# Kernel optimization log

Measured on AMD Instinct MI355X. Metric: run time of the kernel, lower is better.

Reference implementation:

```python
import jax, jax.numpy as jnp
import numpy as np

N = 6144
IN_DIM = 256
HID = 64
HEADS = 4
LAT = 32
ALPHA = 0.2  # LeakyReLU negative slope
NEG_INF = -9e15


def setup_inputs() -> dict:
    key = jax.random.key(0)
    ks = jax.random.split(key, 6)
    x = jax.random.normal(ks[0], (N, IN_DIM), jnp.float32)
    # sparse symmetric 0/1 adjacency, avg degree ~ 25
    A = (jax.random.uniform(ks[1], (N, N)) < 0.004).astype(jnp.float32)
    A = jnp.maximum(A, A.T)
    # xavier-uniform-ish params, matching pyGAT GraphAttentionLayer shapes
    s1 = float(np.sqrt(6.0 / (IN_DIM + HID)))
    W_heads = jax.random.uniform(ks[2], (HEADS, IN_DIM, HID), jnp.float32, -s1, s1)
    sa = float(np.sqrt(6.0 / (2 * HID + 1)))
    a_heads = jax.random.uniform(ks[3], (HEADS, 2 * HID), jnp.float32, -sa, sa)
    s2 = float(np.sqrt(6.0 / (HEADS * HID + LAT)))
    W_out = jax.random.uniform(ks[4], (HEADS * HID, LAT), jnp.float32, -s2, s2)
    sb = float(np.sqrt(6.0 / (2 * LAT + 1)))
    a_out = jax.random.uniform(ks[5], (2 * LAT,), jnp.float32, -sb, sb)
    return {"x": x, "A": A, "W_heads": W_heads, "a_heads": a_heads,
            "W_out": W_out, "a_out": a_out}


def _gat_layer(h, adj_mask, W, a, concat):
    # h: [N, F_in], W: [F_in, F], a: [2F]
    Wh = h @ W                              # [N, F]
    f = W.shape[1]
    e_src = Wh @ a[:f]                      # [N]
    e_dst = Wh @ a[f:]                      # [N]
    e = jax.nn.leaky_relu(e_src[:, None] + e_dst[None, :], ALPHA)  # [N, N]
    e = jnp.where(adj_mask, e, NEG_INF)
    att = jax.nn.softmax(e, axis=1)         # masked softmax over neighbors
    out = att @ Wh                          # [N, F]
    return jax.nn.elu(out) if concat else out


def reference(x, A, W_heads, a_heads, W_out, a_out):
    # normalize(A, 'sym', False): D^{-1/2} A D^{-1/2}
    deg = A.sum(axis=1)
    dinv = jnp.where(deg > 0, deg ** -0.5, 0.0)
    An = A * dinv[:, None] * dinv[None, :]
    mask = An > 0
    heads = [_gat_layer(x, mask, W_heads[i], a_heads[i], True) for i in range(HEADS)]
    h = jnp.concatenate(heads, axis=1)      # [N, HEADS*HID]
    z = jax.nn.elu(_gat_layer(h, mask, W_out, a_out, False))  # [N, LAT]
    return jax.nn.sigmoid(z @ z.T)          # [N, N]
```

## Files before the change

### kernel.cpp

```cpp
#include <hip/hip_runtime.h>
#include <hip/hip_bf16.h>

#define NN 6144
#define IN_DIM 256
#define HID 64
#define HEADS 4
#define LAT 32
#define CAP 192
#define ALPHA 0.2f
#define GEMM_BLOCKS 384

typedef __attribute__((ext_vector_type(8))) short bf16x8;
typedef __attribute__((ext_vector_type(4))) float f32x4;

__device__ __forceinline__ float elu_f(float v)   { return v > 0.f ? v : expm1f(v); }
__device__ __forceinline__ float lrelu_f(float v) { return v > 0.f ? v : ALPHA * v; }

__device__ __forceinline__ void split_bf16(float v, unsigned short& hi, unsigned short& lo) {
    unsigned u = __builtin_bit_cast(unsigned, v);
    hi = (unsigned short)(u >> 16);
    float vh = __builtin_bit_cast(float, u & 0xFFFF0000u);
    float rl = v - vh;
    lo = (unsigned short)(__builtin_bit_cast(unsigned, rl) >> 16);
}
__device__ __forceinline__ unsigned short f2bf(float f) {
    unsigned u = __builtin_bit_cast(unsigned, f);
    return (unsigned short)((u + 0x7FFFu + ((u >> 16) & 1u)) >> 16);
}
__device__ __forceinline__ float bf2f(unsigned short b) {
    return __builtin_bit_cast(float, (unsigned)b << 16);
}

__global__ __launch_bounds__(256) void k_pre(const float* __restrict__ A,
                                             const float* __restrict__ x,
                                             const float* __restrict__ Wheads,
                                             const float* __restrict__ aheads,
                                             int* __restrict__ nbr, int* __restrict__ cnt,
                                             unsigned short* __restrict__ Whb,
                                             float* __restrict__ es, float* __restrict__ ed) {
    __shared__ __align__(16) float smem[2048];
    int bid = blockIdx.x;
    int t = threadIdx.x;
    if (bid < GEMM_BLOCKS) {
        int head = bid & 3, m0 = (bid >> 2) * 64;
        float (*As)[64] = (float(*)[64])smem;
        float (*Bs)[64] = (float(*)[64])(smem + 1024);
        const float* Wc = Wheads + (size_t)head * IN_DIM * HID;
        int ty = t >> 4, tx = t & 15;
        float acc[4][4] = {};
        for (int k0 = 0; k0 < IN_DIM; k0 += 16) {
            {
                int row = t >> 2, k4 = (t & 3) * 4;
                float4 v = *(const float4*)(x + (size_t)(m0 + row) * IN_DIM + k0 + k4);
                As[k4 + 0][row] = v.x; As[k4 + 1][row] = v.y;
                As[k4 + 2][row] = v.z; As[k4 + 3][row] = v.w;
                int kk = t >> 4, n4 = (t & 15) * 4;
                *(float4*)&Bs[kk][n4] = *(const float4*)(Wc + (size_t)(k0 + kk) * HID + n4);
            }
            __syncthreads();
            #pragma unroll
            for (int k = 0; k < 16; ++k) {
                float4 av = *(float4*)&As[k][ty * 4];
                float4 bv = *(float4*)&Bs[k][tx * 4];
                float ar[4] = {av.x, av.y, av.z, av.w};
                float br[4] = {bv.x, bv.y, bv.z, bv.w};
                #pragma unroll
                for (int i = 0; i < 4; ++i)
                    #pragma unroll
                    for (int j = 0; j < 4; ++j)
                        acc[i][j] = fmaf(ar[i], br[j], acc[i][j]);
            }
            __syncthreads();
        }
        #pragma unroll
        for (int i = 0; i < 4; ++i) {
            ushort4 o;
            o.x = f2bf(acc[i][0]); o.y = f2bf(acc[i][1]);
            o.z = f2bf(acc[i][2]); o.w = f2bf(acc[i][3]);
            *(ushort4*)(Whb + (size_t)(m0 + ty * 4 + i) * (HEADS * HID) + head * HID + tx * 4) = o;
        }
        float4 a1v = *(const float4*)(aheads + head * 2 * HID + tx * 4);
        float4 a2v = *(const float4*)(aheads + head * 2 * HID + HID + tx * 4);
        #pragma unroll
        for (int i = 0; i < 4; ++i) {
            float p1 = acc[i][0] * a1v.x + acc[i][1] * a1v.y + acc[i][2] * a1v.z + acc[i][3] * a1v.w;
            float p2 = acc[i][0] * a2v.x + acc[i][1] * a2v.y + acc[i][2] * a2v.z + acc[i][3] * a2v.w;
            #pragma unroll
            for (int off = 8; off; off >>= 1) {
                p1 += __shfl_down(p1, off, 16);
                p2 += __shfl_down(p2, off, 16);
            }
            if (tx == 0) {
                es[head * NN + m0 + ty * 4 + i] = p1;
                ed[head * NN + m0 + ty * 4 + i] = p2;
            }
        }
    } else {
        int row = bid - GEMM_BLOCKS;
        int* lcnt = (int*)smem;
        const float4* Arow = (const float4*)(A + (size_t)row * NN);
        if (t == 0) *lcnt = 0;
        __syncthreads();
        int* my = nbr + (size_t)row * CAP;
        #pragma unroll
        for (int it = 0; it < NN / 4 / 256; ++it) {
            int idx4 = it * 256 + t;
            float4 v = Arow[idx4];
            int base = idx4 * 4;
            if (v.x != 0.f) { int p = atomicAdd(lcnt, 1); if (p < CAP) my[p] = base; }
            if (v.y != 0.f) { int p = atomicAdd(lcnt, 1); if (p < CAP) my[p] = base + 1; }
            if (v.z != 0.f) { int p = atomicAdd(lcnt, 1); if (p < CAP) my[p] = base + 2; }
            if (v.w != 0.f) { int p = atomicAdd(lcnt, 1); if (p < CAP) my[p] = base + 3; }
        }
        __syncthreads();
        if (t == 0) cnt[row] = *lcnt < CAP ? *lcnt : CAP;
    }
}

__global__ __launch_bounds__(256, 8) void k_attn1g2(const int* __restrict__ nbr, const int* __restrict__ cnt,
                                                    const float* __restrict__ es, const float* __restrict__ ed,
                                                    const unsigned short* __restrict__ Whb,
                                                    const float* __restrict__ Wout, const float* __restrict__ aout,
                                                    float* __restrict__ Wh2,
                                                    float* __restrict__ es2, float* __restrict__ ed2) {
    __shared__ int col[CAP];
    __shared__ float att[HEADS][CAP];
    __shared__ float hrow[HEADS * HID];
    __shared__ float part[8][LAT];
    int i = blockIdx.x;
    int t = threadIdx.x, h = t >> 6, l = t & 63;
    int c = cnt[i];
    float hval;
    if (c == 0) {
        float s = 0.f;
        for (int r = 0; r < NN; ++r) s += bf2f(Whb[(size_t)r * (HEADS * HID) + h * HID + l]);
        hval = elu_f(s * (1.0f / NN));
    } else {
        const int* nb = nbr + (size_t)i * CAP;
        float esi = es[h * NN + i];
        float m = -3.0e38f;
        for (int j = l; j < c; j += 64) {
            int cj = nb[j];
            if (h == 0) col[j] = cj;
            float e = lrelu_f(esi + ed[h * NN + cj]);
            att[h][j] = e;
            m = fmaxf(m, e);
        }
        #pragma unroll
        for (int off = 32; off; off >>= 1) m = fmaxf(m, __shfl_down(m, off));
        m = __shfl(m, 0);
        float s = 0.f;
        for (int j = l; j < c; j += 64) {
            float p = __expf(att[h][j] - m);
            att[h][j] = p;
            s += p;
        }
        #pragma unroll
        for (int off = 32; off; off >>= 1) s += __shfl_down(s, off);
        s = __shfl(s, 0);
        __syncthreads();
        float inv = 1.0f / s;
        const unsigned short* WhH = Whb + h * HID + l;
        float a0 = 0.f, a1 = 0.f, a2 = 0.f, a3 = 0.f;
        float a4 = 0.f, a5 = 0.f, a6 = 0.f, a7 = 0.f;
        int j = 0;
        for (; j + 8 <= c; j += 8) {
            a0 = fmaf(att[h][j + 0], bf2f(WhH[(size_t)col[j + 0] * (HEADS * HID)]), a0);
            a1 = fmaf(att[h][j + 1], bf2f(WhH[(size_t)col[j + 1] * (HEADS * HID)]), a1);
            a2 = fmaf(att[h][j + 2], bf2f(WhH[(size_t)col[j + 2] * (HEADS * HID)]), a2);
            a3 = fmaf(att[h][j + 3], bf2f(WhH[(size_t)col[j + 3] * (HEADS * HID)]), a3);
            a4 = fmaf(att[h][j + 4], bf2f(WhH[(size_t)col[j + 4] * (HEADS * HID)]), a4);
            a5 = fmaf(att[h][j + 5], bf2f(WhH[(size_t)col[j + 5] * (HEADS * HID)]), a5);
            a6 = fmaf(att[h][j + 6], bf2f(WhH[(size_t)col[j + 6] * (HEADS * HID)]), a6);
            a7 = fmaf(att[h][j + 7], bf2f(WhH[(size_t)col[j + 7] * (HEADS * HID)]), a7);
        }
        for (; j < c; ++j)
            a0 = fmaf(att[h][j], bf2f(WhH[(size_t)col[j] * (HEADS * HID)]), a0);
        hval = elu_f((((a0 + a1) + (a2 + a3)) + ((a4 + a5) + (a6 + a7))) * inv);
    }
    hrow[h * HID + l] = hval;
    __syncthreads();
    {
        int half = l >> 5, cc = l & 31;
        int tbase = h * HID + half * 32;
        float p = 0.f;
        #pragma unroll 8
        for (int tt = 0; tt < 32; ++tt)
            p = fmaf(hrow[tbase + tt], Wout[(tbase + tt) * LAT + cc], p);
        part[h * 2 + half][cc] = p;
    }
    __syncthreads();
    if (t < 32) {
        float acc = 0.f;
        #pragma unroll
        for (int w = 0; w < 8; ++w) acc += part[w][t];
        Wh2[(size_t)i * LAT + t] = acc;
        float p1 = acc * aout[t], p2 = acc * aout[LAT + t];
        #pragma unroll
        for (int off = 16; off; off >>= 1) {
            p1 += __shfl_down(p1, off, 32);
            p2 += __shfl_down(p2, off, 32);
        }
        if (t == 0) { es2[i] = p1; ed2[i] = p2; }
    }
}

__global__ __launch_bounds__(256, 8) void k_attn2(const int* __restrict__ nbr, const int* __restrict__ cnt,
                                                  const float* __restrict__ es2, const float* __restrict__ ed2,
                                                  const float* __restrict__ Wh2,
                                                  unsigned short* __restrict__ zh, unsigned short* __restrict__ zl) {
    __shared__ float att[4][CAP];
    __shared__ int col[4][CAP];
    int w = threadIdx.x >> 6, l = threadIdx.x & 63;
    int i = blockIdx.x * 4 + w;
    int c = cnt[i];
    if (c == 0) {
        if (l < LAT) {
            float s = 0.f;
            for (int r = 0; r < NN; ++r) s += Wh2[(size_t)r * LAT + l];
            unsigned short hi, lo;
            split_bf16(elu_f(s * (1.0f / NN)), hi, lo);
            zh[(size_t)i * LAT + l] = hi;
            zl[(size_t)i * LAT + l] = lo;
        }
        return;
    }
    float esi = es2[i];
    const int* nb = nbr + (size_t)i * CAP;
    float m = -3.0e38f;
    for (int j = l; j < c; j += 64) {
        int cj = nb[j];
        col[w][j] = cj;
        float e = lrelu_f(esi + ed2[cj]);
        att[w][j] = e;
        m = fmaxf(m, e);
    }
    #pragma unroll
    for (int off = 32; off; off >>= 1) m = fmaxf(m, __shfl_down(m, off));
    m = __shfl(m, 0);
    float s = 0.f;
    for (int j = l; j < c; j += 64) {
        float p = __expf(att[w][j] - m);
        att[w][j] = p;
        s += p;
    }
    #pragma unroll
    for (int off = 32; off; off >>= 1) s += __shfl_down(s, off);
    s = __shfl(s, 0);
    if (l < LAT) {
        float inv = 1.0f / s;
        float a0 = 0.f, a1 = 0.f, a2 = 0.f, a3 = 0.f;
        int j = 0;
        for (; j + 4 <= c; j += 4) {
            a0 = fmaf(att[w][j + 0], Wh2[(size_t)col[w][j + 0] * LAT + l], a0);
            a1 = fmaf(att[w][j + 1], Wh2[(size_t)col[w][j + 1] * LAT + l], a1);
            a2 = fmaf(att[w][j + 2], Wh2[(size_t)col[w][j + 2] * LAT + l], a2);
            a3 = fmaf(att[w][j + 3], Wh2[(size_t)col[w][j + 3] * LAT + l], a3);
        }
        for (; j < c; ++j)
            a0 = fmaf(att[w][j], Wh2[(size_t)col[w][j] * LAT + l], a0);
        unsigned short hi, lo;
        split_bf16(elu_f(((a0 + a1) + (a2 + a3)) * inv), hi, lo);
        zh[(size_t)i * LAT + l] = hi;
        zl[(size_t)i * LAT + l] = lo;
    }
}

__global__ __launch_bounds__(256, 8) void k_zzt(const unsigned short* __restrict__ zh,
                                                const unsigned short* __restrict__ zl,
                                                float* __restrict__ out) {
    int t = threadIdx.x, w = t >> 6, l = t & 63;
    int m0 = blockIdx.y * 64 + w * 16;
    int n0 = blockIdx.x * 64;
    int r = l & 15, kg = (l >> 4) * 8;
    bf16x8 ah = *(const bf16x8*)(zh + (size_t)(m0 + r) * LAT + kg);
    bf16x8 al = *(const bf16x8*)(zl + (size_t)(m0 + r) * LAT + kg);
    int mbase = m0 + (l >> 4) * 4;
    #pragma unroll
    for (int jp = 0; jp < 2; ++jp) {
        int nbA = n0 + (jp * 2 + 0) * 16;
        int nbB = n0 + (jp * 2 + 1) * 16;
        bf16x8 bhA = *(const bf16x8*)(zh + (size_t)(nbA + r) * LAT + kg);
        bf16x8 blA = *(const bf16x8*)(zl + (size_t)(nbA + r) * LAT + kg);
        bf16x8 bhB = *(const bf16x8*)(zh + (size_t)(nbB + r) * LAT + kg);
        bf16x8 blB = *(const bf16x8*)(zl + (size_t)(nbB + r) * LAT + kg);
        f32x4 accA = {0.f, 0.f, 0.f, 0.f};
        accA = __builtin_amdgcn_mfma_f32_16x16x32_bf16(ah, bhA, accA, 0, 0, 0);
        accA = __builtin_amdgcn_mfma_f32_16x16x32_bf16(ah, blA, accA, 0, 0, 0);
        accA = __builtin_amdgcn_mfma_f32_16x16x32_bf16(al, bhA, accA, 0, 0, 0);
        f32x4 accB = {0.f, 0.f, 0.f, 0.f};
        accB = __builtin_amdgcn_mfma_f32_16x16x32_bf16(ah, bhB, accB, 0, 0, 0);
        accB = __builtin_amdgcn_mfma_f32_16x16x32_bf16(ah, blB, accB, 0, 0, 0);
        accB = __builtin_amdgcn_mfma_f32_16x16x32_bf16(al, bhB, accB, 0, 0, 0);
        float4 oA, oB;
        oA.x = 1.0f / (1.0f + __expf(-accA[0]));
        oA.y = 1.0f / (1.0f + __expf(-accA[1]));
        oA.z = 1.0f / (1.0f + __expf(-accA[2]));
        oA.w = 1.0f / (1.0f + __expf(-accA[3]));
        oB.x = 1.0f / (1.0f + __expf(-accB[0]));
        oB.y = 1.0f / (1.0f + __expf(-accB[1]));
        oB.z = 1.0f / (1.0f + __expf(-accB[2]));
        oB.w = 1.0f / (1.0f + __expf(-accB[3]));
        *(float4*)(out + (size_t)(nbA + (l & 15)) * NN + mbase) = oA;
        *(float4*)(out + (size_t)(nbB + (l & 15)) * NN + mbase) = oB;
    }
}

extern "C" void kernel_launch(void* const* d_in, const int* in_sizes, int n_in,
                              void* d_out, int out_size, void* d_ws, size_t ws_size,
                              hipStream_t stream) {
    const float* x      = (const float*)d_in[0];
    const float* A      = (const float*)d_in[1];
    const float* Wheads = (const float*)d_in[2];
    const float* aheads = (const float*)d_in[3];
    const float* Wout   = (const float*)d_in[4];
    const float* aout   = (const float*)d_in[5];
    float* out = (float*)d_out;

    char* ws = (char*)d_ws;
    size_t o = 0;
    auto alloc = [&](size_t bytes) { void* p = ws + o; o += (bytes + 255) & ~(size_t)255; return p; };
    int*   nbr   = (int*)  alloc((size_t)NN * CAP * 4);
    int*   cnt   = (int*)  alloc((size_t)NN * 4);
    unsigned short* Whb = (unsigned short*)alloc((size_t)NN * HEADS * HID * 2);
    float* es    = (float*)alloc((size_t)HEADS * NN * 4);
    float* ed    = (float*)alloc((size_t)HEADS * NN * 4);
    float* Wh2   = (float*)alloc((size_t)NN * LAT * 4);
    float* es2   = (float*)alloc((size_t)NN * 4);
    float* ed2   = (float*)alloc((size_t)NN * 4);
    unsigned short* zh = (unsigned short*)alloc((size_t)NN * LAT * 2);
    unsigned short* zl = (unsigned short*)alloc((size_t)NN * LAT * 2);

    k_pre     <<<GEMM_BLOCKS + NN, 256, 0, stream>>>(A, x, Wheads, aheads, nbr, cnt, Whb, es, ed);
    k_attn1g2 <<<NN, 256, 0, stream>>>(nbr, cnt, es, ed, Whb, Wout, aout, Wh2, es2, ed2);
    k_attn2   <<<NN / 4, 256, 0, stream>>>(nbr, cnt, es2, ed2, Wh2, zh, zl);
    k_zzt     <<<dim3(NN / 64, NN / 64), 256, 0, stream>>>(zh, zl, out);
}
```

Measured before the change: 115.4 us.

## Process one node per wavefront in layer-1 attention with interleaved head scores

The es/ed attention scores are now stored node-major with all four heads together, so one float4 load fetches every head's score for a neighbour. The layer-1 attention kernel now gives each wavefront a whole node (four nodes per block) rather than one block per node. Each lane gathers four consecutive bf16 features per neighbour with a ushort4 load, and the cross-block partial-sum stage for the Wout projection becomes a wave shuffle. This cuts per-node synchronisation and the number of gather instructions, at the cost of a serial 128-term Wout dot product per lane and more shared memory per block.

```diff
diff --git a/kernel.cpp b/kernel.cpp
--- a/kernel.cpp
+++ b/kernel.cpp
@@ -37,7 +37,7 @@
                                              const float* __restrict__ aheads,
                                              int* __restrict__ nbr, int* __restrict__ cnt,
                                              unsigned short* __restrict__ Whb,
-                                             float* __restrict__ es, float* __restrict__ ed) {
+                                             float* __restrict__ es4, float* __restrict__ ed4) {
     __shared__ __align__(16) float smem[2048];
     int bid = blockIdx.x;
     int t = threadIdx.x;
@@ -91,8 +91,8 @@
                 p2 += __shfl_down(p2, off, 16);
             }
             if (tx == 0) {
-                es[head * NN + m0 + ty * 4 + i] = p1;
-                ed[head * NN + m0 + ty * 4 + i] = p2;
+                es4[(size_t)(m0 + ty * 4 + i) * 4 + head] = p1;
+                ed4[(size_t)(m0 + ty * 4 + i) * 4 + head] = p2;
             }
         }
     } else {
@@ -118,90 +118,112 @@
 }
 
 __global__ __launch_bounds__(256, 8) void k_attn1g2(const int* __restrict__ nbr, const int* __restrict__ cnt,
-                                                    const float* __restrict__ es, const float* __restrict__ ed,
+                                                    const float4* __restrict__ es4, const float4* __restrict__ ed4,
                                                     const unsigned short* __restrict__ Whb,
                                                     const float* __restrict__ Wout, const float* __restrict__ aout,
                                                     float* __restrict__ Wh2,
                                                     float* __restrict__ es2, float* __restrict__ ed2) {
-    __shared__ int col[CAP];
-    __shared__ float att[HEADS][CAP];
-    __shared__ float hrow[HEADS * HID];
-    __shared__ float part[8][LAT];
-    int i = blockIdx.x;
-    int t = threadIdx.x, h = t >> 6, l = t & 63;
+    __shared__ int colS[4][CAP];
+    __shared__ __align__(16) float att4[4][CAP][4];
+    __shared__ __align__(16) float hrow[4][HEADS * HID];
+    int w = threadIdx.x >> 6, l = threadIdx.x & 63;
+    int i = blockIdx.x * 4 + w;
     int c = cnt[i];
-    float hval;
+    const int* nb = nbr + (size_t)i * CAP;
+
+    float4 esv = es4[i];
+    float m0 = -3.0e38f, m1 = -3.0e38f, m2 = -3.0e38f, m3 = -3.0e38f;
+    for (int j = l; j < c; j += 64) {
+        int cj = nb[j];
+        colS[w][j] = cj;
+        float4 edv = ed4[cj];
+        float4 e;
+        e.x = lrelu_f(esv.x + edv.x); e.y = lrelu_f(esv.y + edv.y);
+        e.z = lrelu_f(esv.z + edv.z); e.w = lrelu_f(esv.w + edv.w);
+        *(float4*)&att4[w][j][0] = e;
+        m0 = fmaxf(m0, e.x); m1 = fmaxf(m1, e.y);
+        m2 = fmaxf(m2, e.z); m3 = fmaxf(m3, e.w);
+    }
+    #pragma unroll
+    for (int off = 32; off; off >>= 1) {
+        m0 = fmaxf(m0, __shfl_down(m0, off)); m1 = fmaxf(m1, __shfl_down(m1, off));
+        m2 = fmaxf(m2, __shfl_down(m2, off)); m3 = fmaxf(m3, __shfl_down(m3, off));
+    }
+    m0 = __shfl(m0, 0); m1 = __shfl(m1, 0); m2 = __shfl(m2, 0); m3 = __shfl(m3, 0);
+    float s0 = 0.f, s1 = 0.f, s2 = 0.f, s3 = 0.f;
+    for (int j = l; j < c; j += 64) {
+        float4 e = *(float4*)&att4[w][j][0];
+        e.x = __expf(e.x - m0); e.y = __expf(e.y - m1);
+        e.z = __expf(e.z - m2); e.w = __expf(e.w - m3);
+        *(float4*)&att4[w][j][0] = e;
+        s0 += e.x; s1 += e.y; s2 += e.z; s3 += e.w;
+    }
+    #pragma unroll
+    for (int off = 32; off; off >>= 1) {
+        s0 += __shfl_down(s0, off); s1 += __shfl_down(s1, off);
+        s2 += __shfl_down(s2, off); s3 += __shfl_down(s3, off);
+    }
+    s0 = __shfl(s0, 0); s1 = __shfl(s1, 0); s2 = __shfl(s2, 0); s3 = __shfl(s3, 0);
+    __syncthreads();
+
+    int hd = l >> 4;
+    float sh = hd < 2 ? (hd == 0 ? s0 : s1) : (hd == 2 ? s2 : s3);
+    float invh = 1.0f / sh;
+    float4 hv;
     if (c == 0) {
-        float s = 0.f;
-        for (int r = 0; r < NN; ++r) s += bf2f(Whb[(size_t)r * (HEADS * HID) + h * HID + l]);
-        hval = elu_f(s * (1.0f / NN));
+        float a0 = 0.f, a1 = 0.f, a2 = 0.f, a3 = 0.f;
+        for (int r = 0; r < NN; ++r) {
+            ushort4 v = *(const ushort4*)(Whb + (size_t)r * (HEADS * HID) + 4 * l);
+            a0 += bf2f(v.x); a1 += bf2f(v.y); a2 += bf2f(v.z); a3 += bf2f(v.w);
+        }
+        hv.x = elu_f(a0 / NN); hv.y = elu_f(a1 / NN);
+        hv.z = elu_f(a2 / NN); hv.w = elu_f(a3 / NN);
     } else {
-        const int* nb = nbr + (size_t)i * CAP;
-        float esi = es[h * NN + i];
-        float m = -3.0e38f;
-        for (int j = l; j < c; j += 64) {
-            int cj = nb[j];
-            if (h == 0) col[j] = cj;
-            float e = lrelu_f(esi + ed[h * NN + cj]);
-            att[h][j] = e;
-            m = fmaxf(m, e);
-        }
-        #pragma unroll
-        for (int off = 32; off; off >>= 1) m = fmaxf(m, __shfl_down(m, off));
-        m = __shfl(m, 0);
-        float s = 0.f;
-        for (int j = l; j < c; j += 64) {
-            float p = __expf(att[h][j] - m);
-            att[h][j] = p;
-            s += p;
-        }
-        #pragma unroll
-        for (int off = 32; off; off >>= 1) s += __shfl_down(s, off);
-        s = __shfl(s, 0);
-        __syncthreads();
-        float inv = 1.0f / s;
-        const unsigned short* WhH = Whb + h * HID + l;
-        float a0 = 0.f, a1 = 0.f, a2 = 0.f, a3 = 0.f;
-        float a4 = 0.f, a5 = 0.f, a6 = 0.f, a7 = 0.f;
+        const unsigned short* Wb = Whb + 4 * l;
+        float aA0 = 0.f, aA1 = 0.f, aA2 = 0.f, aA3 = 0.f;
+        float aB0 = 0.f, aB1 = 0.f, aB2 = 0.f, aB3 = 0.f;
         int j = 0;
-        for (; j + 8 <= c; j += 8) {
-            a0 = fmaf(att[h][j + 0], bf2f(WhH[(size_t)col[j + 0] * (HEADS * HID)]), a0);
-            a1 = fmaf(att[h][j + 1], bf2f(WhH[(size_t)col[j + 1] * (HEADS * HID)]), a1);
-            a2 = fmaf(att[h][j + 2], bf2f(WhH[(size_t)col[j + 2] * (HEADS * HID)]), a2);
-            a3 = fmaf(att[h][j + 3], bf2f(WhH[(size_t)col[j + 3] * (HEADS * HID)]), a3);
-            a4 = fmaf(att[h][j + 4], bf2f(WhH[(size_t)col[j + 4] * (HEADS * HID)]), a4);
-            a5 = fmaf(att[h][j + 5], bf2f(WhH[(size_t)col[j + 5] * (HEADS * HID)]), a5);
-            a6 = fmaf(att[h][j + 6], bf2f(WhH[(size_t)col[j + 6] * (HEADS * HID)]), a6);
-            a7 = fmaf(att[h][j + 7], bf2f(WhH[(size_t)col[j + 7] * (HEADS * HID)]), a7);
-        }
-        for (; j < c; ++j)
-            a0 = fmaf(att[h][j], bf2f(WhH[(size_t)col[j] * (HEADS * HID)]), a0);
-        hval = elu_f((((a0 + a1) + (a2 + a3)) + ((a4 + a5) + (a6 + a7))) * inv);
-    }
-    hrow[h * HID + l] = hval;
+        for (; j + 2 <= c; j += 2) {
+            int cjA = colS[w][j], cjB = colS[w][j + 1];
+            float fA = att4[w][j][hd], fB = att4[w][j + 1][hd];
+            ushort4 vA = *(const ushort4*)(Wb + (size_t)cjA * (HEADS * HID));
+            ushort4 vB = *(const ushort4*)(Wb + (size_t)cjB * (HEADS * HID));
+            aA0 = fmaf(fA, bf2f(vA.x), aA0); aA1 = fmaf(fA, bf2f(vA.y), aA1);
+            aA2 = fmaf(fA, bf2f(vA.z), aA2); aA3 = fmaf(fA, bf2f(vA.w), aA3);
+            aB0 = fmaf(fB, bf2f(vB.x), aB0); aB1 = fmaf(fB, bf2f(vB.y), aB1);
+            aB2 = fmaf(fB, bf2f(vB.z), aB2); aB3 = fmaf(fB, bf2f(vB.w), aB3);
+        }
+        if (j < c) {
+            int cj = colS[w][j];
+            float f = att4[w][j][hd];
+            ushort4 v = *(const ushort4*)(Wb + (size_t)cj * (HEADS * HID));
+            aA0 = fmaf(f, bf2f(v.x), aA0); aA1 = fmaf(f, bf2f(v.y), aA1);
+            aA2 = fmaf(f, bf2f(v.z), aA2); aA3 = fmaf(f, bf2f(v.w), aA3);
+        }
+        hv.x = elu_f((aA0 + aB0) * invh); hv.y = elu_f((aA1 + aB1) * invh);
+        hv.z = elu_f((aA2 + aB2) * invh); hv.w = elu_f((aA3 + aB3) * invh);
+    }
+    *(float4*)&hrow[w][4 * l] = hv;
     __syncthreads();
+
     {
         int half = l >> 5, cc = l & 31;
-        int tbase = h * HID + half * 32;
+        int tbase = half * 128;
         float p = 0.f;
         #pragma unroll 8
-        for (int tt = 0; tt < 32; ++tt)
-            p = fmaf(hrow[tbase + tt], Wout[(tbase + tt) * LAT + cc], p);
-        part[h * 2 + half][cc] = p;
-    }
-    __syncthreads();
-    if (t < 32) {
-        float acc = 0.f;
-        #pragma unroll
-        for (int w = 0; w < 8; ++w) acc += part[w][t];
-        Wh2[(size_t)i * LAT + t] = acc;
-        float p1 = acc * aout[t], p2 = acc * aout[LAT + t];
-        #pragma unroll
-        for (int off = 16; off; off >>= 1) {
-            p1 += __shfl_down(p1, off, 32);
-            p2 += __shfl_down(p2, off, 32);
-        }
-        if (t == 0) { es2[i] = p1; ed2[i] = p2; }
+        for (int tt = 0; tt < 128; ++tt)
+            p = fmaf(hrow[w][tbase + tt], Wout[(tbase + tt) * LAT + cc], p);
+        p += __shfl_down(p, 32);
+        if (l < 32) {
+            Wh2[(size_t)i * LAT + cc] = p;
+            float p1 = p * aout[cc], p2 = p * aout[LAT + cc];
+            #pragma unroll
+            for (int off = 16; off; off >>= 1) {
+                p1 += __shfl_down(p1, off, 32);
+                p2 += __shfl_down(p2, off, 32);
+            }
+            if (cc == 0) { es2[i] = p1; ed2[i] = p2; }
+        }
     }
 }
 
@@ -323,16 +345,17 @@
     int*   nbr   = (int*)  alloc((size_t)NN * CAP * 4);
     int*   cnt   = (int*)  alloc((size_t)NN * 4);
     unsigned short* Whb = (unsigned short*)alloc((size_t)NN * HEADS * HID * 2);
-    float* es    = (float*)alloc((size_t)HEADS * NN * 4);
-    float* ed    = (float*)alloc((size_t)HEADS * NN * 4);
+    float* es4   = (float*)alloc((size_t)NN * 4 * 4);
+    float* ed4   = (float*)alloc((size_t)NN * 4 * 4);
     float* Wh2   = (float*)alloc((size_t)NN * LAT * 4);
     float* es2   = (float*)alloc((size_t)NN * 4);
     float* ed2   = (float*)alloc((size_t)NN * 4);
     unsigned short* zh = (unsigned short*)alloc((size_t)NN * LAT * 2);
     unsigned short* zl = (unsigned short*)alloc((size_t)NN * LAT * 2);
 
-    k_pre     <<<GEMM_BLOCKS + NN, 256, 0, stream>>>(A, x, Wheads, aheads, nbr, cnt, Whb, es, ed);
-    k_attn1g2 <<<NN, 256, 0, stream>>>(nbr, cnt, es, ed, Whb, Wout, aout, Wh2, es2, ed2);
+    k_pre     <<<GEMM_BLOCKS + NN, 256, 0, stream>>>(A, x, Wheads, aheads, nbr, cnt, Whb, es4, ed4);
+    k_attn1g2 <<<NN / 4, 256, 0, stream>>>(nbr, cnt, (const float4*)es4, (const float4*)ed4,
+                                           Whb, Wout, aout, Wh2, es2, ed2);
     k_attn2   <<<NN / 4, 256, 0, stream>>>(nbr, cnt, es2, ed2, Wh2, zh, zl);
     k_zzt     <<<dim3(NN / 64, NN / 64), 256, 0, stream>>>(zh, zl, out);
 }
```

After: 114.5 us. About the same (-0.8%).
